# Optimization experiments

Hardware: AMD Instinct MI355X
Metric: run time of the kernel (lower is better)

Reference implementation:

```python
import jax, jax.numpy as jnp
import numpy as np

B, D, O, E, H, K = 4096, 1024, 1024, 8, 4096, 2


def setup_inputs() -> dict:
    key = jax.random.key(0)
    ks = jax.random.split(key, 5)
    scale_g = 1.0 / np.sqrt(D)
    scale_1 = 1.0 / np.sqrt(D)
    scale_2 = 1.0 / np.sqrt(H)
    return {
        "x": jax.random.normal(ks[0], (B, D), jnp.float32),
        "gate_w": jax.random.normal(ks[1], (D, E), jnp.float32) * scale_g,
        "gate_b": jnp.zeros((E,), jnp.float32),
        "w1": jax.random.normal(ks[2], (E, D, H), jnp.float32) * scale_1,
        "b1": jnp.zeros((E, H), jnp.float32),
        "w2": jax.random.normal(ks[3], (E, H, O), jnp.float32) * scale_2,
        "b2": jnp.zeros((E, O), jnp.float32),
    }


def reference(x, gate_w, gate_b, w1, b1, w2, b2):
    # Router: top-k logits, softmax over the k selected logits only
    logits = x @ gate_w + gate_b                      # [B, E]
    top_vals, top_idx = jax.lax.top_k(logits, K)      # [B, K]
    routing_w = jax.nn.softmax(top_vals, axis=-1)     # [B, K]

    # Dense all-expert MLP (grouped GEMM), then gather the k selected outputs
    h = jax.nn.relu(jnp.einsum("bd,edh->beh", x, w1) + b1)  # [B, E, H]
    y = jnp.einsum("beh,eho->beo", h, w2) + b2              # [B, E, O]
    sel = jnp.take_along_axis(y, top_idx[:, :, None], axis=1)  # [B, K, O]
    return jnp.sum(routing_w[:, :, None] * sel, axis=1)        # [B, O]
```

## Files before the change

### kernel.cpp

```cpp
#include <hip/hip_runtime.h>
#include <stdint.h>

typedef short bf16x8 __attribute__((ext_vector_type(8)));
typedef float f32x4  __attribute__((ext_vector_type(4)));

constexpr int BT = 4096;
constexpr int DD = 1024;
constexpr int OO = 1024;
constexpr int EE = 8;
constexpr int HH = 4096;

__device__ __forceinline__ unsigned short f2bf(float f) {
  unsigned u = __float_as_uint(f);
  u += 0x7fffu + ((u >> 16) & 1u);
  return (unsigned short)(u >> 16);
}

__device__ __forceinline__ void glds16(const unsigned short* g, unsigned short* l) {
  __builtin_amdgcn_global_load_lds(
      (const __attribute__((address_space(1))) void*)g,
      (__attribute__((address_space(3))) void*)l, 16, 0, 0);
}

__global__ __launch_bounds__(256) void router_k(const float* __restrict__ x,
                                                const float* __restrict__ gw,
                                                const float* __restrict__ gb,
                                                unsigned short* __restrict__ xb,
                                                int* __restrict__ cnt,
                                                int* __restrict__ list,
                                                float* __restrict__ rw) {
  int wave = threadIdx.x >> 6, lane = threadIdx.x & 63;
  int b = blockIdx.x * 4 + wave;
  const float* xrow = x + (size_t)b * DD;
  float acc[8];
#pragma unroll
  for (int e = 0; e < 8; ++e) acc[e] = 0.f;
#pragma unroll
  for (int i = 0; i < 4; ++i) {
    int d0 = i * 256 + lane * 4;
    float4 v = *(const float4*)&xrow[d0];
    unsigned lo = (unsigned)f2bf(v.x) | ((unsigned)f2bf(v.y) << 16);
    unsigned hi = (unsigned)f2bf(v.z) | ((unsigned)f2bf(v.w) << 16);
    *(uint2*)&xb[(size_t)b * DD + d0] = make_uint2(lo, hi);
    const float* g0 = &gw[(size_t)d0 * 8];
    float fv[4] = {v.x, v.y, v.z, v.w};
#pragma unroll
    for (int q = 0; q < 4; ++q) {
      float4 ga = *(const float4*)&g0[q * 8];
      float4 gc = *(const float4*)&g0[q * 8 + 4];
      acc[0] += fv[q] * ga.x; acc[1] += fv[q] * ga.y;
      acc[2] += fv[q] * ga.z; acc[3] += fv[q] * ga.w;
      acc[4] += fv[q] * gc.x; acc[5] += fv[q] * gc.y;
      acc[6] += fv[q] * gc.z; acc[7] += fv[q] * gc.w;
    }
  }
#pragma unroll
  for (int off = 32; off > 0; off >>= 1) {
#pragma unroll
    for (int e = 0; e < 8; ++e) acc[e] += __shfl_down(acc[e], off);
  }
  if (lane == 0) {
    float v[8];
#pragma unroll
    for (int e = 0; e < 8; ++e) v[e] = acc[e] + gb[e];
    int i0 = 0;
#pragma unroll
    for (int e = 1; e < 8; ++e) if (v[e] > v[i0]) i0 = e;
    int i1 = (i0 == 0) ? 1 : 0;
#pragma unroll
    for (int e = 0; e < 8; ++e) if (e != i0 && v[e] > v[i1]) i1 = e;
    float e1 = __expf(v[i1] - v[i0]);
    float inv = 1.0f / (1.0f + e1);
    int p0 = atomicAdd(&cnt[i0], 1);
    list[i0 * BT + p0] = 2 * b;     rw[2 * b]     = inv;
    int p1 = atomicAdd(&cnt[i1], 1);
    list[i1 * BT + p1] = 2 * b + 1; rw[2 * b + 1] = e1 * inv;
  }
}

__global__ void tilemap_k(const int* __restrict__ cnt, int* __restrict__ tmap,
                          int* __restrict__ ntiles) {
  if (threadIdx.x == 0 && blockIdx.x == 0) {
    int t = 0;
    for (int e = 0; e < EE; ++e) {
      int c = cnt[e];
      for (int m0 = 0; m0 < c; m0 += 128) { tmap[2 * t] = e; tmap[2 * t + 1] = m0; ++t; }
    }
    *ntiles = t;
  }
}

__global__ __launch_bounds__(256) void cvt_t_k(const float* __restrict__ src,
                                               unsigned short* __restrict__ dst,
                                               int R, int C) {
  __shared__ unsigned short tile[64][68];
  int e = blockIdx.z;
  const float* s = src + (size_t)e * R * C;
  unsigned short* d = dst + (size_t)e * R * C;
  int r0 = blockIdx.x << 6, c0 = blockIdx.y << 6;
  int t = threadIdx.x;
#pragma unroll
  for (int p = 0; p < 4; ++p) {
    int ch = p * 256 + t;
    int rr = ch >> 4, cc = (ch & 15) << 2;
    float4 v = *(const float4*)&s[(size_t)(r0 + rr) * C + c0 + cc];
    unsigned lo = (unsigned)f2bf(v.x) | ((unsigned)f2bf(v.y) << 16);
    unsigned hi = (unsigned)f2bf(v.z) | ((unsigned)f2bf(v.w) << 16);
    *(uint2*)&tile[rr][cc] = make_uint2(lo, hi);
  }
  __syncthreads();
#pragma unroll
  for (int p = 0; p < 4; ++p) {
    int ch = p * 256 + t;
    int cc = ch >> 4, rr = (ch & 15) << 2;
    unsigned short v0 = tile[rr + 0][cc];
    unsigned short v1 = tile[rr + 1][cc];
    unsigned short v2 = tile[rr + 2][cc];
    unsigned short v3 = tile[rr + 3][cc];
    unsigned lo = (unsigned)v0 | ((unsigned)v1 << 16);
    unsigned hi = (unsigned)v2 | ((unsigned)v3 << 16);
    *(uint2*)&d[(size_t)(c0 + cc) * R + r0 + rr] = make_uint2(lo, hi);
  }
}

__global__ __launch_bounds__(256, 3) void gemm1_k(const unsigned short* __restrict__ xb,
                                                  const unsigned short* __restrict__ w1t,
                                                  const float* __restrict__ b1,
                                                  const int* __restrict__ cnt,
                                                  const int* __restrict__ list,
                                                  const int* __restrict__ tmap,
                                                  const int* __restrict__ ntiles,
                                                  unsigned short* __restrict__ h) {
  int ti = blockIdx.x;
  if (ti >= *ntiles) return;
  int e = tmap[2 * ti], m0 = tmap[2 * ti + 1];
  int cnt_e = cnt[e];
  int n0 = blockIdx.y * 128;

  __shared__ int slotbuf[128];
  __shared__ __align__(16) unsigned short Ash[128 * 64];
  __shared__ __align__(16) unsigned short Bsh[128 * 64];

  int t = threadIdx.x;
  if (t < 128) {
    int r = m0 + t;
    slotbuf[t] = list[e * BT + (r < cnt_e ? r : 0)];
  }
  __syncthreads();

  int w = t >> 6, l = t & 63;
  int lm = l & 15, lq = l >> 4;
  int wm = (w & 1) * 64, wn = (w >> 1) * 64;

  const unsigned short* Bsrc = w1t + (size_t)e * HH * DD + (size_t)n0 * DD;

  const unsigned short* aS[4];
  const unsigned short* bS[4];
  unsigned short* aL[4];
  unsigned short* bL[4];
#pragma unroll
  for (int j = 0; j < 4; ++j) {
    int idx = 4 * w + j;
    int row = idx * 8 + (l >> 3);
    int koff = (l & 7) * 8;
    int tok = slotbuf[row] >> 1;
    aS[j] = xb + (size_t)tok * DD + koff;
    bS[j] = Bsrc + (size_t)row * DD + koff;
    aL[j] = &Ash[idx * 512];
    bL[j] = &Bsh[idx * 512];
  }

  f32x4 acc[4][4];
#pragma unroll
  for (int mi = 0; mi < 4; ++mi)
#pragma unroll
    for (int ni = 0; ni < 4; ++ni) acc[mi][ni] = f32x4{0.f, 0.f, 0.f, 0.f};

  for (int k0 = 0; k0 < DD; k0 += 64) {
#pragma unroll
    for (int j = 0; j < 4; ++j) glds16(aS[j] + k0, aL[j]);
#pragma unroll
    for (int j = 0; j < 4; ++j) glds16(bS[j] + k0, bL[j]);
    __syncthreads();
#pragma unroll
    for (int ks = 0; ks < 2; ++ks) {
      bf16x8 af[4], bfr[4];
      int kb = ks * 32 + lq * 8;
#pragma unroll
      for (int mi = 0; mi < 4; ++mi)
        af[mi] = *(const bf16x8*)&Ash[(wm + mi * 16 + lm) * 64 + kb];
#pragma unroll
      for (int ni = 0; ni < 4; ++ni)
        bfr[ni] = *(const bf16x8*)&Bsh[(wn + ni * 16 + lm) * 64 + kb];
#pragma unroll
      for (int mi = 0; mi < 4; ++mi)
#pragma unroll
        for (int ni = 0; ni < 4; ++ni)
          acc[mi][ni] = __builtin_amdgcn_mfma_f32_16x16x32_bf16(af[mi], bfr[ni], acc[mi][ni], 0, 0, 0);
    }
    __syncthreads();
  }

#pragma unroll
  for (int ni = 0; ni < 4; ++ni) {
    int ncol = n0 + wn + ni * 16 + lm;
    float bias = b1[e * HH + ncol];
#pragma unroll
    for (int mi = 0; mi < 4; ++mi) {
      int mbase = wm + mi * 16 + lq * 4;
#pragma unroll
      for (int r = 0; r < 4; ++r) {
        int mrow = mbase + r;
        if (m0 + mrow < cnt_e) {
          float v = fmaxf(acc[mi][ni][r] + bias, 0.0f);
          h[(size_t)slotbuf[mrow] * HH + ncol] = f2bf(v);
        }
      }
    }
  }
}

__global__ __launch_bounds__(256, 3) void gemm2_k(const unsigned short* __restrict__ h,
                                                  const unsigned short* __restrict__ w2t,
                                                  const float* __restrict__ b2,
                                                  const int* __restrict__ cnt,
                                                  const int* __restrict__ list,
                                                  const int* __restrict__ tmap,
                                                  const int* __restrict__ ntiles,
                                                  const float* __restrict__ rw,
                                                  float* __restrict__ out) {
  int ti = blockIdx.x;
  if (ti >= *ntiles) return;
  int e = tmap[2 * ti], m0 = tmap[2 * ti + 1];
  int cnt_e = cnt[e];
  int n0 = blockIdx.y * 128;
  int kb0 = blockIdx.z * (HH / 4);

  __shared__ int slotbuf[128];
  __shared__ float rwbuf[128];
  __shared__ __align__(16) unsigned short Ash[128 * 64];
  __shared__ __align__(16) unsigned short Bsh[128 * 64];

  int t = threadIdx.x;
  if (t < 128) {
    int r = m0 + t;
    int s_ = list[e * BT + (r < cnt_e ? r : 0)];
    slotbuf[t] = s_;
    rwbuf[t] = rw[s_];
  }
  __syncthreads();

  int w = t >> 6, l = t & 63;
  int lm = l & 15, lq = l >> 4;
  int wm = (w & 1) * 64, wn = (w >> 1) * 64;

  const unsigned short* Bsrc = w2t + (size_t)e * OO * HH + (size_t)n0 * HH;

  const unsigned short* aS[4];
  const unsigned short* bS[4];
  unsigned short* aL[4];
  unsigned short* bL[4];
#pragma unroll
  for (int j = 0; j < 4; ++j) {
    int idx = 4 * w + j;
    int row = idx * 8 + (l >> 3);
    int koff = (l & 7) * 8;
    int slot = slotbuf[row];
    aS[j] = h + (size_t)slot * HH + kb0 + koff;
    bS[j] = Bsrc + (size_t)row * HH + kb0 + koff;
    aL[j] = &Ash[idx * 512];
    bL[j] = &Bsh[idx * 512];
  }

  f32x4 acc[4][4];
#pragma unroll
  for (int mi = 0; mi < 4; ++mi)
#pragma unroll
    for (int ni = 0; ni < 4; ++ni) acc[mi][ni] = f32x4{0.f, 0.f, 0.f, 0.f};

  for (int k0 = 0; k0 < HH / 4; k0 += 64) {
#pragma unroll
    for (int j = 0; j < 4; ++j) glds16(aS[j] + k0, aL[j]);
#pragma unroll
    for (int j = 0; j < 4; ++j) glds16(bS[j] + k0, bL[j]);
    __syncthreads();
#pragma unroll
    for (int ks = 0; ks < 2; ++ks) {
      bf16x8 af[4], bfr[4];
      int kb = ks * 32 + lq * 8;
#pragma unroll
      for (int mi = 0; mi < 4; ++mi)
        af[mi] = *(const bf16x8*)&Ash[(wm + mi * 16 + lm) * 64 + kb];
#pragma unroll
      for (int ni = 0; ni < 4; ++ni)
        bfr[ni] = *(const bf16x8*)&Bsh[(wn + ni * 16 + lm) * 64 + kb];
#pragma unroll
      for (int mi = 0; mi < 4; ++mi)
#pragma unroll
        for (int ni = 0; ni < 4; ++ni)
          acc[mi][ni] = __builtin_amdgcn_mfma_f32_16x16x32_bf16(af[mi], bfr[ni], acc[mi][ni], 0, 0, 0);
    }
    __syncthreads();
  }

  bool addbias = (blockIdx.z == 0);
#pragma unroll
  for (int ni = 0; ni < 4; ++ni) {
    int ncol = n0 + wn + ni * 16 + lm;
    float bias = addbias ? b2[e * OO + ncol] : 0.0f;
#pragma unroll
    for (int mi = 0; mi < 4; ++mi) {
      int mbase = wm + mi * 16 + lq * 4;
#pragma unroll
      for (int r = 0; r < 4; ++r) {
        int mrow = mbase + r;
        if (m0 + mrow < cnt_e) {
          float v = (acc[mi][ni][r] + bias) * rwbuf[mrow];
          int slot = slotbuf[mrow];
          atomicAdd(&out[(size_t)(slot >> 1) * OO + ncol], v);
        }
      }
    }
  }
}

extern "C" void kernel_launch(void* const* d_in, const int* in_sizes, int n_in,
                              void* d_out, int out_size, void* d_ws, size_t ws_size,
                              hipStream_t stream) {
  const float* x  = (const float*)d_in[0];
  const float* gw = (const float*)d_in[1];
  const float* gb = (const float*)d_in[2];
  const float* w1 = (const float*)d_in[3];
  const float* b1 = (const float*)d_in[4];
  const float* w2 = (const float*)d_in[5];
  const float* b2 = (const float*)d_in[6];
  float* out = (float*)d_out;
  char* ws = (char*)d_ws;

  int*            cnt    = (int*)(ws);
  int*            list   = (int*)(ws + 1024);
  float*          rw     = (float*)(ws + (256u << 10));
  int*            tmap   = (int*)(ws + (512u << 10));
  int*            ntiles = (int*)(ws + (520u << 10));
  unsigned short* xb     = (unsigned short*)(ws + (1u  << 20));
  unsigned short* wt     = (unsigned short*)(ws + (16u << 20));
  unsigned short* h      = (unsigned short*)(ws + (88u << 20));
  size_t need = (88u << 20) + (size_t)2 * BT * HH * 2;
  if (ws_size < need) return;

  hipMemsetAsync(cnt, 0, 1024, stream);
  hipMemsetAsync(out, 0, (size_t)BT * OO * sizeof(float), stream);

  router_k<<<BT / 4, 256, 0, stream>>>(x, gw, gb, xb, cnt, list, rw);
  tilemap_k<<<1, 64, 0, stream>>>(cnt, tmap, ntiles);
  cvt_t_k<<<dim3(DD / 64, HH / 64, EE), 256, 0, stream>>>(w1, wt, DD, HH);
  gemm1_k<<<dim3(72, HH / 128), 256, 0, stream>>>(xb, wt, b1, cnt, list, tmap, ntiles, h);
  cvt_t_k<<<dim3(HH / 64, OO / 64, EE), 256, 0, stream>>>(w2, wt, HH, OO);
  gemm2_k<<<dim3(72, OO / 128, 4), 256, 0, stream>>>(h, wt, b2, cnt, list, tmap, ntiles, rw, out);
}
```

Baseline: 752.7 us.

## Compact expert-sorted hidden buffer, swap grid axes, replace atomics with split-K buffer and combine

```diff
diff --git a/kernel.cpp b/kernel.cpp
--- a/kernel.cpp
+++ b/kernel.cpp
@@ -9,6 +9,7 @@
 constexpr int OO = 1024;
 constexpr int EE = 8;
 constexpr int HH = 4096;
+constexpr int SLOTS = 2 * BT;
 
 __device__ __forceinline__ unsigned short f2bf(float f) {
   unsigned u = __float_as_uint(f);
@@ -81,10 +82,13 @@
 __global__ void tilemap_k(const int* __restrict__ cnt, int* __restrict__ tmap,
                           int* __restrict__ ntiles) {
   if (threadIdx.x == 0 && blockIdx.x == 0) {
-    int t = 0;
+    int t = 0, basewalk = 0;
     for (int e = 0; e < EE; ++e) {
       int c = cnt[e];
-      for (int m0 = 0; m0 < c; m0 += 128) { tmap[2 * t] = e; tmap[2 * t + 1] = m0; ++t; }
+      for (int m0 = 0; m0 < c; m0 += 128) {
+        tmap[4 * t] = e; tmap[4 * t + 1] = m0; tmap[4 * t + 2] = basewalk + m0; ++t;
+      }
+      basewalk += c;
     }
     *ntiles = t;
   }
@@ -93,7 +97,7 @@
 __global__ __launch_bounds__(256) void cvt_t_k(const float* __restrict__ src,
                                                unsigned short* __restrict__ dst,
                                                int R, int C) {
-  __shared__ unsigned short tile[64][68];
+  __shared__ unsigned short tile[64][66];
   int e = blockIdx.z;
   const float* s = src + (size_t)e * R * C;
   unsigned short* d = dst + (size_t)e * R * C;
@@ -123,19 +127,19 @@
   }
 }
 
-__global__ __launch_bounds__(256, 3) void gemm1_k(const unsigned short* __restrict__ xb,
+__global__ __launch_bounds__(256, 4) void gemm1_k(const unsigned short* __restrict__ xb,
                                                   const unsigned short* __restrict__ w1t,
                                                   const float* __restrict__ b1,
                                                   const int* __restrict__ cnt,
                                                   const int* __restrict__ list,
                                                   const int* __restrict__ tmap,
                                                   const int* __restrict__ ntiles,
-                                                  unsigned short* __restrict__ h) {
-  int ti = blockIdx.x;
+                                                  unsigned short* __restrict__ hc) {
+  int ti = blockIdx.y;
   if (ti >= *ntiles) return;
-  int e = tmap[2 * ti], m0 = tmap[2 * ti + 1];
+  int e = tmap[4 * ti], m0 = tmap[4 * ti + 1], base = tmap[4 * ti + 2];
   int cnt_e = cnt[e];
-  int n0 = blockIdx.y * 128;
+  int n0 = blockIdx.x * 128;
 
   __shared__ int slotbuf[128];
   __shared__ __align__(16) unsigned short Ash[128 * 64];
@@ -213,14 +217,14 @@
         int mrow = mbase + r;
         if (m0 + mrow < cnt_e) {
           float v = fmaxf(acc[mi][ni][r] + bias, 0.0f);
-          h[(size_t)slotbuf[mrow] * HH + ncol] = f2bf(v);
+          hc[(size_t)(base + mrow) * HH + ncol] = f2bf(v);
         }
       }
     }
   }
 }
 
-__global__ __launch_bounds__(256, 3) void gemm2_k(const unsigned short* __restrict__ h,
+__global__ __launch_bounds__(256, 4) void gemm2_k(const unsigned short* __restrict__ hc,
                                                   const unsigned short* __restrict__ w2t,
                                                   const float* __restrict__ b2,
                                                   const int* __restrict__ cnt,
@@ -228,13 +232,15 @@
                                                   const int* __restrict__ tmap,
                                                   const int* __restrict__ ntiles,
                                                   const float* __restrict__ rw,
+                                                  float* __restrict__ ybuf,
                                                   float* __restrict__ out) {
-  int ti = blockIdx.x;
+  int ti = blockIdx.y;
   if (ti >= *ntiles) return;
-  int e = tmap[2 * ti], m0 = tmap[2 * ti + 1];
+  int e = tmap[4 * ti], m0 = tmap[4 * ti + 1], base = tmap[4 * ti + 2];
   int cnt_e = cnt[e];
-  int n0 = blockIdx.y * 128;
-  int kb0 = blockIdx.z * (HH / 4);
+  int n0 = blockIdx.x * 128;
+  int ksl = HH / gridDim.z;
+  int kb0 = blockIdx.z * ksl;
 
   __shared__ int slotbuf[128];
   __shared__ float rwbuf[128];
@@ -265,8 +271,7 @@
     int idx = 4 * w + j;
     int row = idx * 8 + (l >> 3);
     int koff = (l & 7) * 8;
-    int slot = slotbuf[row];
-    aS[j] = h + (size_t)slot * HH + kb0 + koff;
+    aS[j] = hc + (size_t)(base + row) * HH + kb0 + koff;
     bS[j] = Bsrc + (size_t)row * HH + kb0 + koff;
     aL[j] = &Ash[idx * 512];
     bL[j] = &Bsh[idx * 512];
@@ -278,7 +283,7 @@
 #pragma unroll
     for (int ni = 0; ni < 4; ++ni) acc[mi][ni] = f32x4{0.f, 0.f, 0.f, 0.f};
 
-  for (int k0 = 0; k0 < HH / 4; k0 += 64) {
+  for (int k0 = 0; k0 < ksl; k0 += 64) {
 #pragma unroll
     for (int j = 0; j < 4; ++j) glds16(aS[j] + k0, aL[j]);
 #pragma unroll
@@ -304,6 +309,7 @@
   }
 
   bool addbias = (blockIdx.z == 0);
+  size_t ybase = (size_t)blockIdx.z * SLOTS;
 #pragma unroll
   for (int ni = 0; ni < 4; ++ni) {
     int ncol = n0 + wn + ni * 16 + lm;
@@ -317,11 +323,27 @@
         if (m0 + mrow < cnt_e) {
           float v = (acc[mi][ni][r] + bias) * rwbuf[mrow];
           int slot = slotbuf[mrow];
-          atomicAdd(&out[(size_t)(slot >> 1) * OO + ncol], v);
+          if (ybuf) ybuf[(ybase + slot) * OO + ncol] = v;
+          else      atomicAdd(&out[(size_t)(slot >> 1) * OO + ncol], v);
         }
       }
     }
   }
+}
+
+__global__ __launch_bounds__(256) void combine_k(const float* __restrict__ y,
+                                                 float* __restrict__ out, int nz) {
+  int i = blockIdx.x * 256 + threadIdx.x;
+  int b = i >> 8, c = i & 255;
+  f32x4 acc = {0.f, 0.f, 0.f, 0.f};
+  for (int z = 0; z < nz; ++z) {
+#pragma unroll
+    for (int k = 0; k < 2; ++k) {
+      const float4 v = *(const float4*)&y[((size_t)z * SLOTS + 2 * b + k) * OO + c * 4];
+      acc[0] += v.x; acc[1] += v.y; acc[2] += v.z; acc[3] += v.w;
+    }
+  }
+  *(f32x4*)&out[(size_t)b * OO + c * 4] = acc;
 }
 
 extern "C" void kernel_launch(void* const* d_in, const int* in_sizes, int n_in,
@@ -338,23 +360,32 @@
   char* ws = (char*)d_ws;
 
   int*            cnt    = (int*)(ws);
-  int*            list   = (int*)(ws + 1024);
-  float*          rw     = (float*)(ws + (256u << 10));
-  int*            tmap   = (int*)(ws + (512u << 10));
-  int*            ntiles = (int*)(ws + (520u << 10));
+  int*            ntiles = (int*)(ws + 64);
+  int*            tmap   = (int*)(ws + 128);
+  float*          rw     = (float*)(ws + 4096);
+  int*            list   = (int*)(ws + (64u << 10));
   unsigned short* xb     = (unsigned short*)(ws + (1u  << 20));
-  unsigned short* wt     = (unsigned short*)(ws + (16u << 20));
-  unsigned short* h      = (unsigned short*)(ws + (88u << 20));
-  size_t need = (88u << 20) + (size_t)2 * BT * HH * 2;
-  if (ws_size < need) return;
-
-  hipMemsetAsync(cnt, 0, 1024, stream);
-  hipMemsetAsync(out, 0, (size_t)BT * OO * sizeof(float), stream);
+  unsigned short* wt     = (unsigned short*)(ws + (9u  << 20));
+  unsigned short* hc     = (unsigned short*)(ws + (73u << 20));
+  float*          ybuf   = (float*)(ws + (138u << 20));
+
+  size_t need_min = (138u << 20);
+  if (ws_size < need_min) return;
+  int zsplit;
+  float* ypass;
+  if (ws_size >= (138u << 20) + (size_t)2 * SLOTS * OO * 4) { zsplit = 2; ypass = ybuf; }
+  else if (ws_size >= (138u << 20) + (size_t)SLOTS * OO * 4) { zsplit = 1; ypass = ybuf; }
+  else { zsplit = 2; ypass = nullptr; }
+
+  hipMemsetAsync(cnt, 0, 64, stream);
+  if (!ypass) hipMemsetAsync(out, 0, (size_t)BT * OO * sizeof(float), stream);
 
   router_k<<<BT / 4, 256, 0, stream>>>(x, gw, gb, xb, cnt, list, rw);
   tilemap_k<<<1, 64, 0, stream>>>(cnt, tmap, ntiles);
   cvt_t_k<<<dim3(DD / 64, HH / 64, EE), 256, 0, stream>>>(w1, wt, DD, HH);
-  gemm1_k<<<dim3(72, HH / 128), 256, 0, stream>>>(xb, wt, b1, cnt, list, tmap, ntiles, h);
+  gemm1_k<<<dim3(HH / 128, 72), 256, 0, stream>>>(xb, wt, b1, cnt, list, tmap, ntiles, hc);
   cvt_t_k<<<dim3(HH / 64, OO / 64, EE), 256, 0, stream>>>(w2, wt, HH, OO);
-  gemm2_k<<<dim3(72, OO / 128, 4), 256, 0, stream>>>(h, wt, b2, cnt, list, tmap, ntiles, rw, out);
-}
+  gemm2_k<<<dim3(OO / 128, 72, zsplit), 256, 0, stream>>>(hc, wt, b2, cnt, list, tmap, ntiles, rw, ypass, out);
+  if (ypass)
+    combine_k<<<BT * OO / 1024, 256, 0, stream>>>(ybuf, out, zsplit);
+}
```

Measured after the change: 718.9 us. -4.5%, faster.
